# Kernel tuning notes

Measured on AMD Instinct MI355X. Metric: run time of the kernel, lower is better.

Reference implementation:

```python
import jax, jax.numpy as jnp
import numpy as np
import math

B, N, D, RANK = 16, 65536, 8, 2
IN_SIZE, OUT_SIZE = 4096, 4096
TWO_PI = 2.0 * math.pi


def setup_inputs() -> dict:
    key = jax.random.key(0)
    k = jax.random.split(key, 6)
    x = jax.random.normal(k[0], (B, IN_SIZE), jnp.float32)
    # means live in index space: dim0 in [0, OUT_SIZE), dim1 in [0, IN_SIZE)
    means = jax.random.uniform(k[1], (B, N, RANK), jnp.float32) * jnp.array(
        [OUT_SIZE - 1, IN_SIZE - 1], jnp.float32)
    sigmas = jax.random.uniform(k[2], (B, N), jnp.float32) * 2.0 + 0.5  # positive stddevs
    values = jax.random.normal(k[3], (B, N), jnp.float32)
    bias = jax.random.normal(k[4], (OUT_SIZE,), jnp.float32) * 0.1
    noise = jax.random.normal(k[5], (B, N, D, RANK), jnp.float32)  # reparam noise (torch.randn in sample())
    return {"x": x, "means": means, "sigmas": sigmas, "values": values,
            "bias": bias, "noise": noise}


def reference(x, means, sigmas, values, bias, noise):
    # --- sample(): d reparameterized MVN samples per (mean, sigma) -> [B,N,D,RANK]
    samples = noise * sigmas[:, :, None, None] + means[:, :, None, :]
    # --- densities(): isotropic Gaussian pdf of samples under their own MVN -> [B,N,D]
    diff = samples - means[:, :, None, :]
    products = jnp.sum(diff * diff, axis=-1)              # squared distances [B,N,D]
    s2 = (sigmas * sigmas)[:, :, None]                    # sigma^2, [B,N,1]
    den = jnp.sqrt((TWO_PI ** RANK) * s2 ** RANK)
    probs = jnp.exp(-products / (2.0 * s2)) / den         # [B,N,D]
    # normalize proportions over the D samples of each tuple
    probs = probs / jnp.sum(probs, axis=2, keepdims=True)
    # --- round and clamp to integer indices in w_shape = (OUT_SIZE, IN_SIZE)
    upper = jnp.array([OUT_SIZE - 1, IN_SIZE - 1], jnp.float32)
    ints = jnp.clip(jnp.round(samples), 0.0, upper).astype(jnp.int32)  # [B,N,D,2]
    # --- weighted values, flattened to N*D sparse entries per batch element
    vals = (values[:, :, None] * probs).reshape(B, N * D)
    out_idx = ints[..., 0].reshape(B, N * D)
    in_idx = ints[..., 1].reshape(B, N * D)
    # --- segmented sparse matvec: y[b, o] += vals * x[b, i]
    # (equivalent to the sorted grouped dot-product loop in the torch code)
    def one(xb, oi, ii, vb):
        return jnp.zeros((OUT_SIZE,), x.dtype).at[oi].add(vb * xb[ii])
    y = jax.vmap(one)(x, out_idx, in_idx, vals)           # [B, OUT_SIZE]
    return y + bias
```

## Files before the change

kernel.cpp:

```cpp
#include <hip/hip_runtime.h>
#include <math.h>

#define BB 16
#define NN 65536
#define DD 8
#define OUT_SIZE 4096
#define IN_SIZE 4096

#define BLOCKS_PER_B 32
#define NC (NN / BLOCKS_PER_B)
#define BLOCK_THREADS 1024

__global__ void init_out(const float* __restrict__ bias, float* __restrict__ y) {
    int i = blockIdx.x * blockDim.x + threadIdx.x;
    y[i] = bias[i & (OUT_SIZE - 1)];
}

__global__ __launch_bounds__(BLOCK_THREADS, 8)
void hyper_scatter(const float* __restrict__ x,
                   const float* __restrict__ means,
                   const float* __restrict__ sigmas,
                   const float* __restrict__ values,
                   const float* __restrict__ noise,
                   float* __restrict__ y) {
    __shared__ float ys[OUT_SIZE];

    const int b     = blockIdx.x / BLOCKS_PER_B;
    const int chunk = blockIdx.x % BLOCKS_PER_B;
    const int tid   = threadIdx.x;
    const float* xb = x + (size_t)b * IN_SIZE;

    {
        float4* ydst = (float4*)ys;
        if (tid < OUT_SIZE / 4) {
            ydst[tid] = make_float4(0.f, 0.f, 0.f, 0.f);
        }
    }
    __syncthreads();

    const int n0 = chunk * NC;
    #pragma unroll
    for (int nl = tid; nl < NC; nl += BLOCK_THREADS) {
        const size_t base = (size_t)b * NN + (size_t)(n0 + nl);
        const float2 mean  = ((const float2*)means)[base];
        const float  sigma = sigmas[base];
        const float  value = values[base];

        const float4* np4 = (const float4*)(noise + base * (size_t)(DD * 2));
        float4 nz0 = np4[0], nz1 = np4[1], nz2 = np4[2], nz3 = np4[3];
        float nr[DD * 2] = { nz0.x, nz0.y, nz0.z, nz0.w,
                             nz1.x, nz1.y, nz1.z, nz1.w,
                             nz2.x, nz2.y, nz2.z, nz2.w,
                             nz3.x, nz3.y, nz3.z, nz3.w };

        const float neg_inv_2s2 = -0.5f / (sigma * sigma);

        float p[DD];
        int   oi[DD], ii[DD];
        float psum = 0.f;
        #pragma unroll
        for (int d = 0; d < DD; ++d) {
            float s0 = __fadd_rn(__fmul_rn(nr[2 * d],     sigma), mean.x);
            float s1 = __fadd_rn(__fmul_rn(nr[2 * d + 1], sigma), mean.y);
            float d0 = s0 - mean.x;
            float d1 = s1 - mean.y;
            float q  = d0 * d0 + d1 * d1;
            float pd = __expf(q * neg_inv_2s2);
            p[d] = pd;
            psum += pd;
            oi[d] = (int)fminf(fmaxf(rintf(s0), 0.f), (float)(OUT_SIZE - 1));
            ii[d] = (int)fminf(fmaxf(rintf(s1), 0.f), (float)(IN_SIZE - 1));
        }

        float xv[DD];
        #pragma unroll
        for (int d = 0; d < DD; ++d) xv[d] = xb[ii[d]];

        const float wscale = value / psum;
        #pragma unroll
        for (int d = 0; d < DD; ++d) {
            atomicAdd(&ys[oi[d]], wscale * p[d] * xv[d]);
        }
    }
    __syncthreads();

    float* yb = y + (size_t)b * OUT_SIZE;
    #pragma unroll
    for (int o = tid; o < OUT_SIZE; o += BLOCK_THREADS) {
        unsafeAtomicAdd(&yb[o], ys[o]);
    }
}

extern "C" void kernel_launch(void* const* d_in, const int* in_sizes, int n_in,
                              void* d_out, int out_size, void* d_ws, size_t ws_size,
                              hipStream_t stream) {
    const float* x      = (const float*)d_in[0];
    const float* means  = (const float*)d_in[1];
    const float* sigmas = (const float*)d_in[2];
    const float* values = (const float*)d_in[3];
    const float* bias   = (const float*)d_in[4];
    const float* noise  = (const float*)d_in[5];
    float* y = (float*)d_out;

    init_out<<<(BB * OUT_SIZE) / 256, 256, 0, stream>>>(bias, y);
    hyper_scatter<<<BB * BLOCKS_PER_B, BLOCK_THREADS, 0, stream>>>(
        x, means, sigmas, values, noise, y);
}
```

Baseline: 144.1 us.

## Split each tuple across four lanes with dedup of duplicate indices and prefetch

Each tuple's eight samples are now handled by four cooperating lanes, two samples per lane. Noise is read with one coalesced float4 per lane instead of four strided float4 loads per thread. The lanes reduce the probability sum through shuffles, merge samples that land on the same (out,in) index before the shared atomic add, and register-prefetch the next iteration's inputs. This is meant to improve memory coalescing and cut LDS atomic contention, in exchange for many extra shuffles and compare/select instructions per sample.

New measurement: 148.8 us. 1.03x slower.

```diff
diff --git a/kernel.cpp b/kernel.cpp
--- a/kernel.cpp
+++ b/kernel.cpp
@@ -10,6 +10,8 @@
 #define BLOCKS_PER_B 32
 #define NC (NN / BLOCKS_PER_B)
 #define BLOCK_THREADS 1024
+#define TUPLES_PER_ITER (BLOCK_THREADS/4)
+#define NITER (NC / TUPLES_PER_ITER)
 
 __global__ void init_out(const float* __restrict__ bias, float* __restrict__ y) {
     int i = blockIdx.x * blockDim.x + threadIdx.x;
@@ -28,59 +30,82 @@
     const int b     = blockIdx.x / BLOCKS_PER_B;
     const int chunk = blockIdx.x % BLOCKS_PER_B;
     const int tid   = threadIdx.x;
+    const int q     = tid & 3;
     const float* xb = x + (size_t)b * IN_SIZE;
 
-    {
-        float4* ydst = (float4*)ys;
-        if (tid < OUT_SIZE / 4) {
-            ydst[tid] = make_float4(0.f, 0.f, 0.f, 0.f);
-        }
-    }
+    ((float4*)ys)[tid] = make_float4(0.f, 0.f, 0.f, 0.f);
     __syncthreads();
 
     const int n0 = chunk * NC;
-    #pragma unroll
-    for (int nl = tid; nl < NC; nl += BLOCK_THREADS) {
-        const size_t base = (size_t)b * NN + (size_t)(n0 + nl);
-        const float2 mean  = ((const float2*)means)[base];
-        const float  sigma = sigmas[base];
-        const float  value = values[base];
+    const size_t tb = (size_t)b * NN + n0;
 
-        const float4* np4 = (const float4*)(noise + base * (size_t)(DD * 2));
-        float4 nz0 = np4[0], nz1 = np4[1], nz2 = np4[2], nz3 = np4[3];
-        float nr[DD * 2] = { nz0.x, nz0.y, nz0.z, nz0.w,
-                             nz1.x, nz1.y, nz1.z, nz1.w,
-                             nz2.x, nz2.y, nz2.z, nz2.w,
-                             nz3.x, nz3.y, nz3.z, nz3.w };
+    float4 nz   = ((const float4*)noise)[(tb + 0) * 4 + tid];
+    float2 mean = ((const float2*)means)[tb + (tid >> 2)];
+    float  sigma = sigmas[tb + (tid >> 2)];
+    float  value = values[tb + (tid >> 2)];
+
+    for (int it = 0; it < NITER; ++it) {
+        float4 nz_n; float2 mean_n; float sigma_n, value_n;
+        if (it + 1 < NITER) {
+            const size_t tn = tb + (size_t)(it + 1) * TUPLES_PER_ITER;
+            nz_n    = ((const float4*)noise)[tn * 4 + tid];
+            mean_n  = ((const float2*)means)[tn + (tid >> 2)];
+            sigma_n = sigmas[tn + (tid >> 2)];
+            value_n = values[tn + (tid >> 2)];
+        }
 
         const float neg_inv_2s2 = -0.5f / (sigma * sigma);
+        float sA0 = __fadd_rn(__fmul_rn(nz.x, sigma), mean.x);
+        float sA1 = __fadd_rn(__fmul_rn(nz.y, sigma), mean.y);
+        float sB0 = __fadd_rn(__fmul_rn(nz.z, sigma), mean.x);
+        float sB1 = __fadd_rn(__fmul_rn(nz.w, sigma), mean.y);
+        float dA0 = sA0 - mean.x, dA1 = sA1 - mean.y;
+        float dB0 = sB0 - mean.x, dB1 = sB1 - mean.y;
+        float pA = __expf((dA0 * dA0 + dA1 * dA1) * neg_inv_2s2);
+        float pB = __expf((dB0 * dB0 + dB1 * dB1) * neg_inv_2s2);
+        int oiA = (int)fminf(fmaxf(rintf(sA0), 0.f), (float)(OUT_SIZE - 1));
+        int iiA = (int)fminf(fmaxf(rintf(sA1), 0.f), (float)(IN_SIZE - 1));
+        int oiB = (int)fminf(fmaxf(rintf(sB0), 0.f), (float)(OUT_SIZE - 1));
+        int iiB = (int)fminf(fmaxf(rintf(sB1), 0.f), (float)(IN_SIZE - 1));
+        int kA = (oiA << 12) | iiA;
+        int kB = (oiB << 12) | iiB;
 
-        float p[DD];
-        int   oi[DD], ii[DD];
-        float psum = 0.f;
-        #pragma unroll
-        for (int d = 0; d < DD; ++d) {
-            float s0 = __fadd_rn(__fmul_rn(nr[2 * d],     sigma), mean.x);
-            float s1 = __fadd_rn(__fmul_rn(nr[2 * d + 1], sigma), mean.y);
-            float d0 = s0 - mean.x;
-            float d1 = s1 - mean.y;
-            float q  = d0 * d0 + d1 * d1;
-            float pd = __expf(q * neg_inv_2s2);
-            p[d] = pd;
-            psum += pd;
-            oi[d] = (int)fminf(fmaxf(rintf(s0), 0.f), (float)(OUT_SIZE - 1));
-            ii[d] = (int)fminf(fmaxf(rintf(s1), 0.f), (float)(IN_SIZE - 1));
-        }
+        float pAB = pA + pB;
+        float t1  = pAB + __shfl_xor(pAB, 1, 4);
+        float psum = t1 + __shfl_xor(t1, 2, 4);
+        const float wscale = value / psum;
 
-        float xv[DD];
-        #pragma unroll
-        for (int d = 0; d < DD; ++d) xv[d] = xb[ii[d]];
+        int   kA1 = __shfl_xor(kA, 1, 4), kB1 = __shfl_xor(kB, 1, 4);
+        float pA1 = __shfl_xor(pA, 1, 4), pB1 = __shfl_xor(pB, 1, 4);
+        int   kA2 = __shfl_xor(kA, 2, 4), kB2 = __shfl_xor(kB, 2, 4);
+        float pA2 = __shfl_xor(pA, 2, 4), pB2 = __shfl_xor(pB, 2, 4);
+        int   kA3 = __shfl_xor(kA, 3, 4), kB3 = __shfl_xor(kB, 3, 4);
+        float pA3 = __shfl_xor(pA, 3, 4), pB3 = __shfl_xor(pB, 3, 4);
+        bool e1 = (q ^ 1) < q, e2 = (q ^ 2) < q, e3 = (q ^ 3) < q;
 
-        const float wscale = value / psum;
-        #pragma unroll
-        for (int d = 0; d < DD; ++d) {
-            atomicAdd(&ys[oi[d]], wscale * p[d] * xv[d]);
-        }
+        bool deadA = (e1 && (kA1 == kA || kB1 == kA))
+                  || (e2 && (kA2 == kA || kB2 == kA))
+                  || (e3 && (kA3 == kA || kB3 == kA));
+        float wA = pA + ((kB == kA) ? pB : 0.f)
+                 + (!e1 ? ((kA1 == kA ? pA1 : 0.f) + (kB1 == kA ? pB1 : 0.f)) : 0.f)
+                 + (!e2 ? ((kA2 == kA ? pA2 : 0.f) + (kB2 == kA ? pB2 : 0.f)) : 0.f)
+                 + (!e3 ? ((kA3 == kA ? pA3 : 0.f) + (kB3 == kA ? pB3 : 0.f)) : 0.f);
+        bool deadB = (kA == kB)
+                  || (e1 && (kA1 == kB || kB1 == kB))
+                  || (e2 && (kA2 == kB || kB2 == kB))
+                  || (e3 && (kA3 == kB || kB3 == kB));
+        float wB = pB
+                 + (!e1 ? ((kA1 == kB ? pA1 : 0.f) + (kB1 == kB ? pB1 : 0.f)) : 0.f)
+                 + (!e2 ? ((kA2 == kB ? pA2 : 0.f) + (kB2 == kB ? pB2 : 0.f)) : 0.f)
+                 + (!e3 ? ((kA3 == kB ? pA3 : 0.f) + (kB3 == kB ? pB3 : 0.f)) : 0.f);
+
+        float xvA = 0.f, xvB = 0.f;
+        if (!deadA) xvA = xb[iiA];
+        if (!deadB) xvB = xb[iiB];
+        if (!deadA) atomicAdd(&ys[oiA], wscale * wA * xvA);
+        if (!deadB) atomicAdd(&ys[oiB], wscale * wB * xvB);
+
+        nz = nz_n; mean = mean_n; sigma = sigma_n; value = value_n;
     }
     __syncthreads();
 
```
